# Kernel tuning notes

Hardware: AMD Instinct MI355X
Metric: run time of the kernel (lower is better)

The kernel has to match this reference:

```python
import math
import jax, jax.numpy as jnp
import numpy as np

L, H, D, FF, V, S = 12, 12, 768, 3072, 32000, 1024
HD = D // H
EPS = 1e-5
B, T = 2, 1024


def layernorm(x, w, b):
    mu = jnp.mean(x, axis=-1, keepdims=True)
    var = jnp.mean(jnp.square(x - mu), axis=-1, keepdims=True)
    return (x - mu) * jax.lax.rsqrt(var + EPS) * w + b


def setup_inputs() -> dict:
    key = jax.random.key(0)
    ks = jax.random.split(key, 12)
    std = 0.02
    std_res = 0.02 / math.sqrt(2 * L)  # out_proj / down_proj scaled init
    return {
        "input_ids": jax.random.randint(ks[0], (B, T), 0, V),
        "tok_emb": jax.random.normal(ks[1], (V, D), jnp.float32) * std,
        "pos_emb": jax.random.normal(ks[2], (S, D), jnp.float32) * std,
        "ln1_w": jnp.ones((L, D), jnp.float32),
        "ln1_b": jnp.zeros((L, D), jnp.float32),
        "qkv_w": jax.random.normal(ks[3], (L, 3 * D, D), jnp.float32) * std,
        "out_w": jax.random.normal(ks[4], (L, D, D), jnp.float32) * std_res,
        "ln2_w": jnp.ones((L, D), jnp.float32),
        "ln2_b": jnp.zeros((L, D), jnp.float32),
        "up_w": jax.random.normal(ks[5], (L, FF, D), jnp.float32) * std,
        "down_w": jax.random.normal(ks[6], (L, D, FF), jnp.float32) * std_res,
        "lnf_w": jnp.ones((D,), jnp.float32),
        "lnf_b": jnp.zeros((D,), jnp.float32),
    }


def reference(input_ids, tok_emb, pos_emb, ln1_w, ln1_b, qkv_w, out_w,
              ln2_w, ln2_b, up_w, down_w, lnf_w, lnf_b):
    b, t = input_ids.shape
    x = tok_emb[input_ids] + pos_emb[:t]  # (B,T,D); dropout = eval no-op
    causal = jnp.tril(jnp.ones((t, t), bool))  # (T,T)
    scale = 1.0 / math.sqrt(HD)

    def block(x, p):
        l1w, l1b, qkvw, ow, l2w, l2b, uw, dw = p
        h = layernorm(x, l1w, l1b)
        qkv = h @ qkvw.T  # (B,T,3D)
        q, k, v = jnp.split(qkv, 3, axis=-1)
        q = q.reshape(b, t, H, HD)
        k = k.reshape(b, t, H, HD)
        v = v.reshape(b, t, H, HD)
        scores = jnp.einsum('bihd,bjhd->bhij', q, k) * scale
        scores = jnp.where(causal, scores, -jnp.inf)
        probs = jax.nn.softmax(scores, axis=-1)  # attn_dropout = eval no-op
        o = jnp.einsum('bhij,bjhd->bihd', probs, v).reshape(b, t, D)
        x = x + o @ ow.T
        h2 = layernorm(x, l2w, l2b)
        x = x + jax.nn.gelu(h2 @ uw.T, approximate=False) @ dw.T
        return x, None

    x, _ = jax.lax.scan(block, x, (ln1_w, ln1_b, qkv_w, out_w, ln2_w, ln2_b, up_w, down_w))
    x = layernorm(x, lnf_w, lnf_b)
    logits = x @ tok_emb.T  # tied lm_head
    return logits
```

## Files before the change

### kernel.cpp

```cpp
#include <hip/hip_runtime.h>
#include <hip/hip_bf16.h>
#include <math.h>

#define L_  12
#define H_  12
#define D_  768
#define FF_ 3072
#define V_  32000
#define T_  1024
#define B_  2
#define BT_ (B_*T_)

typedef unsigned short ushort_t;
typedef unsigned int   uint_t;
typedef __bf16 bf16x8 __attribute__((ext_vector_type(8)));
typedef float  f32x4  __attribute__((ext_vector_type(4)));

__device__ __forceinline__ uint_t f2bf1(float f) {
    uint_t u = __builtin_bit_cast(uint_t, f);
    return (u + 0x7FFFu + ((u >> 16) & 1u)) >> 16;
}
__device__ __forceinline__ uint_t f2bf2(float lo, float hi) {
    return f2bf1(lo) | (f2bf1(hi) << 16);
}

__device__ __forceinline__ void gl_lds16(const ushort_t* g, ushort_t* l) {
    __builtin_amdgcn_global_load_lds(
        (const __attribute__((address_space(1))) uint_t*)g,
        (__attribute__((address_space(3))) uint_t*)l, 16, 0, 0);
}

__global__ __launch_bounds__(256) void cast_bf16(const float* __restrict__ in,
                                                 ushort_t* __restrict__ out, int n8)
{
    for (int i = blockIdx.x * 256 + threadIdx.x; i < n8; i += gridDim.x * 256) {
        const float4* p = (const float4*)(in + (size_t)i * 8);
        float4 a = p[0], b = p[1];
        *(uint4*)(out + (size_t)i * 8) =
            make_uint4(f2bf2(a.x,a.y), f2bf2(a.z,a.w), f2bf2(b.x,b.y), f2bf2(b.z,b.w));
    }
}

__global__ __launch_bounds__(256) void cast_layer(const float* __restrict__ q,
    const float* __restrict__ o, const float* __restrict__ u, const float* __restrict__ d,
    ushort_t* __restrict__ out)
{
    const int N0 = 3*D_*D_/8, N1 = N0 + D_*D_/8, N2 = N1 + FF_*D_/8, N3 = N2 + D_*FF_/8;
    for (int i = blockIdx.x * 256 + threadIdx.x; i < N3; i += gridDim.x * 256) {
        const float* src;
        if      (i < N0) src = q + (size_t)i * 8;
        else if (i < N1) src = o + (size_t)(i - N0) * 8;
        else if (i < N2) src = u + (size_t)(i - N1) * 8;
        else             src = d + (size_t)(i - N2) * 8;
        const float4* p = (const float4*)src;
        float4 a = p[0], b = p[1];
        *(uint4*)(out + (size_t)i * 8) =
            make_uint4(f2bf2(a.x,a.y), f2bf2(a.z,a.w), f2bf2(b.x,b.y), f2bf2(b.z,b.w));
    }
}

#define EPI_F32   0
#define EPI_BF16  1
#define EPI_GELU  2
#define EPI_ATOM  3

template <int EPI, int KS>
__global__ __launch_bounds__(256) void gemm_bt(
    const ushort_t* __restrict__ A, const ushort_t* __restrict__ W,
    void* __restrict__ Cv, int N, int K, int Kc)
{
    __shared__ ushort_t As[128 * 64];
    __shared__ ushort_t Bs[128 * 64];

    const int tid  = threadIdx.x;
    const int w    = tid >> 6;
    const int lane = tid & 63;

    const int nwg = gridDim.x;
    int swz = (blockIdx.x & 7) * (nwg >> 3) + (blockIdx.x >> 3);
    const int mt   = swz & 15;
    int rest       = swz >> 4;
    const int ks   = rest & (KS - 1);
    const int nt   = rest / KS;
    const int m0 = mt * 128, n0 = nt * 128;
    const int kb = ks * Kc,  ke = kb + Kc;

    const int srow = lane >> 3;
    const int scol = ((lane & 7) ^ srow) * 8;
    const ushort_t* gA = A + (size_t)(m0 + w * 32 + srow) * K + scol;
    const ushort_t* gW = W + (size_t)(n0 + w * 32 + srow) * K + scol;
    ushort_t* lA = As + w * 2048;
    ushort_t* lB = Bs + w * 2048;
    const size_t row8 = (size_t)8 * K;

    const int lr = lane & 15;
    const int lg = lane >> 4;
    const int wm = (w >> 1) * 64;
    const int wn = (w & 1) * 64;

    f32x4 acc[4][4] = {};

    for (int k0 = kb; k0 < ke; k0 += 64) {
        #pragma unroll
        for (int i = 0; i < 4; ++i) {
            gl_lds16(gA + k0 + i * row8, lA + i * 512);
            gl_lds16(gW + k0 + i * row8, lB + i * 512);
        }
        __syncthreads();

        #pragma unroll
        for (int kk = 0; kk < 2; ++kk) {
            bf16x8 av[4], bv[4];
            #pragma unroll
            for (int i = 0; i < 4; ++i) {
                int rr = wm + i * 16 + lr;
                int ch = (lg + 4 * kk) ^ (rr & 7);
                av[i] = *(const bf16x8*)&As[rr * 64 + ch * 8];
            }
            #pragma unroll
            for (int j = 0; j < 4; ++j) {
                int rr = wn + j * 16 + lr;
                int ch = (lg + 4 * kk) ^ (rr & 7);
                bv[j] = *(const bf16x8*)&Bs[rr * 64 + ch * 8];
            }
            #pragma unroll
            for (int i = 0; i < 4; ++i)
                #pragma unroll
                for (int j = 0; j < 4; ++j)
                    acc[i][j] = __builtin_amdgcn_mfma_f32_16x16x32_bf16(av[i], bv[j], acc[i][j], 0, 0, 0);
        }
        __syncthreads();
    }

    float*    Cf = (float*)Cv;
    ushort_t* Cb = (ushort_t*)Cv;
    const int rbase = (lane >> 4) * 4;
    #pragma unroll
    for (int i = 0; i < 4; ++i) {
        #pragma unroll
        for (int j = 0; j < 4; ++j) {
            #pragma unroll
            for (int r = 0; r < 4; ++r) {
                int row = m0 + wm + i * 16 + rbase + r;
                int col = n0 + wn + j * 16 + lr;
                size_t idx = (size_t)row * N + col;
                float v = acc[i][j][r];
                if (EPI == EPI_F32)  Cf[idx] = v;
                if (EPI == EPI_BF16) Cb[idx] = (ushort_t)f2bf1(v);
                if (EPI == EPI_GELU) Cb[idx] = (ushort_t)f2bf1(0.5f * v * (1.0f + erff(v * 0.70710678118654752f)));
                if (EPI == EPI_ATOM) atomicAdd(&Cf[idx], v);
            }
        }
    }
}

__global__ __launch_bounds__(256) void vprep(const ushort_t* __restrict__ qkv,
                                             ushort_t* __restrict__ vt)
{
    __shared__ ushort_t Vs[64][72];
    const int blk   = blockIdx.x;
    const int ttile = blk & 15;
    const int bh    = blk >> 4;
    const int b     = bh / H_;
    const int h     = bh % H_;
    const int tid   = threadIdx.x;
    const int t0    = ttile * 64;
    {
        const int tr = tid >> 2;
        const int dc = (tid & 3) * 16;
        const uint4* src = (const uint4*)(qkv + (size_t)(b * T_ + t0 + tr) * 2304 + 1536 + h * 64 + dc);
        uint4 v0 = src[0], v1 = src[1];
        *(uint4*)&Vs[tr][dc]     = v0;
        *(uint4*)&Vs[tr][dc + 8] = v1;
    }
    __syncthreads();
    {
        const int d  = tid >> 2;
        const int jc = (tid & 3) * 16;
        uint_t w[8];
        #pragma unroll
        for (int i = 0; i < 8; ++i)
            w[i] = (uint_t)Vs[jc + 2*i][d] | ((uint_t)Vs[jc + 2*i + 1][d] << 16);
        uint4* dst = (uint4*)(vt + ((size_t)bh * 64 + d) * T_ + t0 + jc);
        dst[0] = make_uint4(w[0], w[1], w[2], w[3]);
        dst[1] = make_uint4(w[4], w[5], w[6], w[7]);
    }
}

__global__ __launch_bounds__(64) void attn_mfma(const ushort_t* __restrict__ qkv,
    const ushort_t* __restrict__ vt, ushort_t* __restrict__ o)
{
    __shared__ ushort_t Ps[16 * 136];

    int swz = (blockIdx.x & 7) * 192 + (blockIdx.x >> 3);
    const int bh  = swz >> 6;
    const int qtl = 63 - (swz & 63);
    const int b   = bh / H_;
    const int h   = bh % H_;
    const int lane = threadIdx.x;
    const int l15  = lane & 15;
    const int lg   = lane >> 4;
    const int qbase = qtl * 16;
    const int qlast = qbase + 15;

    const ushort_t* qp = qkv + ((size_t)(b * T_) + qbase + l15) * 2304 + h * 64 + lg * 8;
    bf16x8 qf0 = *(const bf16x8*)qp;
    bf16x8 qf1 = *(const bf16x8*)(qp + 32);

    f32x4 od[4] = {};
    float mr[4] = {-INFINITY, -INFINITY, -INFINITY, -INFINITY};
    float lr[4] = {0.f, 0.f, 0.f, 0.f};

    const ushort_t* kbase = qkv + (size_t)(b * T_) * 2304 + 768 + h * 64;
    const ushort_t* vbase = vt + (size_t)bh * 64 * T_;
    const float SC = 0.18033688011112042f;

    for (int j0 = 0; j0 <= qlast; j0 += 128) {
        f32x4 s[8];
        __builtin_amdgcn_s_setprio(1);
        #pragma unroll
        for (int n = 0; n < 8; ++n) {
            if (j0 + 16 * n <= qlast) {
                const ushort_t* kr = kbase + (size_t)(j0 + 16 * n + l15) * 2304 + lg * 8;
                bf16x8 kf0 = *(const bf16x8*)kr;
                bf16x8 kf1 = *(const bf16x8*)(kr + 32);
                f32x4 a = {};
                a = __builtin_amdgcn_mfma_f32_16x16x32_bf16(qf0, kf0, a, 0, 0, 0);
                a = __builtin_amdgcn_mfma_f32_16x16x32_bf16(qf1, kf1, a, 0, 0, 0);
                s[n] = a;
            } else {
                s[n] = f32x4{-INFINITY, -INFINITY, -INFINITY, -INFINITY};
            }
        }
        __builtin_amdgcn_s_setprio(0);

        #pragma unroll
        for (int n = 0; n < 8; ++n) {
            #pragma unroll
            for (int r = 0; r < 4; ++r) {
                float v = s[n][r] * SC;
                int jg = j0 + 16 * n + l15;
                int qg = qbase + lg * 4 + r;
                if (jg > qg) v = -INFINITY;
                s[n][r] = v;
            }
        }

        float al[4];
        #pragma unroll
        for (int r = 0; r < 4; ++r) {
            float tm = fmaxf(fmaxf(fmaxf(s[0][r], s[1][r]), fmaxf(s[2][r], s[3][r])),
                             fmaxf(fmaxf(s[4][r], s[5][r]), fmaxf(s[6][r], s[7][r])));
            tm = fmaxf(tm, __shfl_xor(tm, 1, 64));
            tm = fmaxf(tm, __shfl_xor(tm, 2, 64));
            tm = fmaxf(tm, __shfl_xor(tm, 4, 64));
            tm = fmaxf(tm, __shfl_xor(tm, 8, 64));
            float mn = fmaxf(mr[r], tm);
            al[r] = exp2f(mr[r] - mn);
            mr[r] = mn;
        }
        #pragma unroll
        for (int n = 0; n < 8; ++n)
            #pragma unroll
            for (int r = 0; r < 4; ++r)
                s[n][r] = exp2f(s[n][r] - mr[r]);
        #pragma unroll
        for (int r = 0; r < 4; ++r) {
            float ps = (s[0][r] + s[1][r]) + (s[2][r] + s[3][r]);
            ps += (s[4][r] + s[5][r]) + (s[6][r] + s[7][r]);
            ps += __shfl_xor(ps, 1, 64);
            ps += __shfl_xor(ps, 2, 64);
            ps += __shfl_xor(ps, 4, 64);
            ps += __shfl_xor(ps, 8, 64);
            lr[r] = lr[r] * al[r] + ps;
        }
        #pragma unroll
        for (int n = 0; n < 4; ++n)
            #pragma unroll
            for (int r = 0; r < 4; ++r)
                od[n][r] *= al[r];

        #pragma unroll
        for (int n = 0; n < 8; ++n)
            #pragma unroll
            for (int r = 0; r < 4; ++r)
                Ps[(lg * 4 + r) * 136 + 16 * n + l15] = (ushort_t)f2bf1(s[n][r]);

        __builtin_amdgcn_s_setprio(1);
        #pragma unroll
        for (int kc = 0; kc < 4; ++kc) {
            if (j0 + kc * 32 <= qlast) {
                bf16x8 pa = *(const bf16x8*)&Ps[l15 * 136 + kc * 32 + lg * 8];
                #pragma unroll
                for (int nn = 0; nn < 4; ++nn) {
                    bf16x8 vf = *(const bf16x8*)&vbase[(size_t)(16 * nn + l15) * T_ + j0 + kc * 32 + lg * 8];
                    od[nn] = __builtin_amdgcn_mfma_f32_16x16x32_bf16(pa, vf, od[nn], 0, 0, 0);
                }
            }
        }
        __builtin_amdgcn_s_setprio(0);
    }

    #pragma unroll
    for (int r = 0; r < 4; ++r) {
        float inv = 1.0f / lr[r];
        int row = qbase + lg * 4 + r;
        ushort_t* op = o + ((size_t)(b * T_ + row)) * 768 + h * 64 + l15;
        #pragma unroll
        for (int nn = 0; nn < 4; ++nn)
            op[16 * nn] = (ushort_t)f2bf1(od[nn][r] * inv);
    }
}

__global__ __launch_bounds__(256) void ln_kernel(const float* __restrict__ x,
    const float* __restrict__ w, const float* __restrict__ bia, ushort_t* __restrict__ out)
{
    const int row = blockIdx.x;
    const int tid = threadIdx.x;
    const float* xr = x + (size_t)row * 768;
    float v0 = xr[tid], v1 = xr[tid + 256], v2 = xr[tid + 512];
    float s  = v0 + v1 + v2;
    float s2 = v0 * v0 + v1 * v1 + v2 * v2;
    #pragma unroll
    for (int off = 32; off > 0; off >>= 1) {
        s  += __shfl_down(s,  off, 64);
        s2 += __shfl_down(s2, off, 64);
    }
    __shared__ float sh[8];
    const int wave = tid >> 6;
    if ((tid & 63) == 0) { sh[wave] = s; sh[4 + wave] = s2; }
    __syncthreads();
    float S  = sh[0] + sh[1] + sh[2] + sh[3];
    float S2 = sh[4] + sh[5] + sh[6] + sh[7];
    float mean = S * (1.f / 768.f);
    float var  = S2 * (1.f / 768.f) - mean * mean;
    float inv  = rsqrtf(var + 1e-5f);
    ushort_t* orow = out + (size_t)row * 768;
    orow[tid]       = (ushort_t)f2bf1((v0 - mean) * inv * w[tid]       + bia[tid]);
    orow[tid + 256] = (ushort_t)f2bf1((v1 - mean) * inv * w[tid + 256] + bia[tid + 256]);
    orow[tid + 512] = (ushort_t)f2bf1((v2 - mean) * inv * w[tid + 512] + bia[tid + 512]);
}

__global__ __launch_bounds__(256) void embed_kernel(const int* __restrict__ ids,
    const float* __restrict__ tok, const float* __restrict__ pos, float* __restrict__ x)
{
    const int bt = blockIdx.x;
    const int t  = bt % T_;
    const int id = ids[bt];
    const int tid = threadIdx.x;
    const float* tr = tok + (size_t)id * 768;
    const float* pr = pos + (size_t)t * 768;
    float* xr = x + (size_t)bt * 768;
    xr[tid]       = tr[tid]       + pr[tid];
    xr[tid + 256] = tr[tid + 256] + pr[tid + 256];
    xr[tid + 512] = tr[tid + 512] + pr[tid + 512];
}

extern "C" void kernel_launch(void* const* d_in, const int* in_sizes, int n_in,
                              void* d_out, int out_size, void* d_ws, size_t ws_size,
                              hipStream_t stream)
{
    const int*   ids   = (const int*)  d_in[0];
    const float* tok   = (const float*)d_in[1];
    const float* pos   = (const float*)d_in[2];
    const float* ln1w  = (const float*)d_in[3];
    const float* ln1b  = (const float*)d_in[4];
    const float* qkvw  = (const float*)d_in[5];
    const float* outw  = (const float*)d_in[6];
    const float* ln2w  = (const float*)d_in[7];
    const float* ln2b  = (const float*)d_in[8];
    const float* upw   = (const float*)d_in[9];
    const float* downw = (const float*)d_in[10];
    const float* lnfw  = (const float*)d_in[11];
    const float* lnfb  = (const float*)d_in[12];
    float* out = (float*)d_out;

    char* ws = (char*)d_ws;
    ushort_t* h    = (ushort_t*)ws;
    float*    x    = (float*)   (ws + 3145728);
    ushort_t* qkv  = (ushort_t*)(ws + 9437184);
    ushort_t* o    = qkv  + (size_t)BT_ * 3 * D_;
    ushort_t* vt   = o    + (size_t)BT_ * D_;
    ushort_t* ffh  = vt   + (size_t)B_ * H_ * 64 * T_;
    ushort_t* layerW = ffh + (size_t)BT_ * FF_;
    ushort_t* tokW = (ushort_t*)(ws + 3145728);

    ushort_t* qkvwB  = layerW;
    ushort_t* outwB  = qkvwB + (size_t)3 * D_ * D_;
    ushort_t* upwB   = outwB + (size_t)D_ * D_;
    ushort_t* downwB = upwB  + (size_t)FF_ * D_;

    embed_kernel<<<BT_, 256, 0, stream>>>(ids, tok, pos, x);

    for (int l = 0; l < L_; ++l) {
        cast_layer<<<1024, 256, 0, stream>>>(
            qkvw  + (size_t)l * 3 * D_ * D_,
            outw  + (size_t)l * D_ * D_,
            upw   + (size_t)l * FF_ * D_,
            downw + (size_t)l * D_ * FF_, layerW);

        ln_kernel<<<BT_, 256, 0, stream>>>(x, ln1w + l * D_, ln1b + l * D_, h);

        gemm_bt<EPI_BF16, 1><<<16 * (3 * D_ / 128), 256, 0, stream>>>(
            h, qkvwB, qkv, 3 * D_, D_, D_);

        vprep<<<B_ * H_ * (T_ / 64), 256, 0, stream>>>(qkv, vt);
        attn_mfma<<<B_ * H_ * (T_ / 16), 64, 0, stream>>>(qkv, vt, o);

        gemm_bt<EPI_ATOM, 2><<<16 * (D_ / 128) * 2, 256, 0, stream>>>(
            o, outwB, x, D_, D_, D_ / 2);

        ln_kernel<<<BT_, 256, 0, stream>>>(x, ln2w + l * D_, ln2b + l * D_, h);

        gemm_bt<EPI_GELU, 1><<<16 * (FF_ / 128), 256, 0, stream>>>(
            h, upwB, ffh, FF_, D_, D_);

        gemm_bt<EPI_ATOM, 4><<<16 * (D_ / 128) * 4, 256, 0, stream>>>(
            ffh, downwB, x, D_, FF_, FF_ / 4);
    }

    ln_kernel<<<BT_, 256, 0, stream>>>(x, lnfw, lnfb, h);
    cast_bf16<<<2048, 256, 0, stream>>>(tok, tokW, V_ * D_ / 8);
    gemm_bt<EPI_F32, 1><<<16 * (V_ / 128), 256, 0, stream>>>(
        h, tokW, out, V_, D_, D_);
}
```

Before: 2.195 ms.

## Double-buffer GEMM LDS tiles and replace split-K atomics with BM=64 residual epilogue

The GEMM kernel now double-buffers its LDS tiles, so the next K-slice is prefetched while MFMAs run on the current one. It also raises wave priority around the MFMA block. The out-projection and down-projection GEMMs drop split-K with atomicAdd and instead use a 64-row M tile with a plain residual-add store, which keeps enough workgroups in flight. This removes atomic traffic and the serialized load-then-compute pattern, at the cost of twice the LDS per block and one fewer wave of split-K parallelism on the long-K down-projection.

```diff
diff --git a/kernel.cpp b/kernel.cpp
--- a/kernel.cpp
+++ b/kernel.cpp
@@ -62,15 +62,18 @@
 #define EPI_F32   0
 #define EPI_BF16  1
 #define EPI_GELU  2
-#define EPI_ATOM  3
-
-template <int EPI, int KS>
+#define EPI_RES   3
+
+template <int EPI, int BM>
 __global__ __launch_bounds__(256) void gemm_bt(
     const ushort_t* __restrict__ A, const ushort_t* __restrict__ W,
-    void* __restrict__ Cv, int N, int K, int Kc)
-{
-    __shared__ ushort_t As[128 * 64];
-    __shared__ ushort_t Bs[128 * 64];
+    const float* R, void* Cv, int N, int K)
+{
+    constexpr int MI = BM / 32;
+    constexpr int AH = BM * 64;
+    constexpr int BH = 128 * 64;
+    __shared__ ushort_t As[2 * AH];
+    __shared__ ushort_t Bs[2 * BH];
 
     const int tid  = threadIdx.x;
     const int w    = tid >> 6;
@@ -78,65 +81,74 @@
 
     const int nwg = gridDim.x;
     int swz = (blockIdx.x & 7) * (nwg >> 3) + (blockIdx.x >> 3);
-    const int mt   = swz & 15;
-    int rest       = swz >> 4;
-    const int ks   = rest & (KS - 1);
-    const int nt   = rest / KS;
-    const int m0 = mt * 128, n0 = nt * 128;
-    const int kb = ks * Kc,  ke = kb + Kc;
+    constexpr int MT = 2048 / BM;
+    const int mt = swz & (MT - 1);
+    const int nt = swz / MT;
+    const int m0 = mt * BM, n0 = nt * 128;
 
     const int srow = lane >> 3;
     const int scol = ((lane & 7) ^ srow) * 8;
-    const ushort_t* gA = A + (size_t)(m0 + w * 32 + srow) * K + scol;
+    const ushort_t* gA = A + (size_t)(m0 + w * (BM / 4) + srow) * K + scol;
     const ushort_t* gW = W + (size_t)(n0 + w * 32 + srow) * K + scol;
-    ushort_t* lA = As + w * 2048;
-    ushort_t* lB = Bs + w * 2048;
     const size_t row8 = (size_t)8 * K;
 
     const int lr = lane & 15;
     const int lg = lane >> 4;
-    const int wm = (w >> 1) * 64;
+    const int wm = (w >> 1) * (BM / 2);
     const int wn = (w & 1) * 64;
 
-    f32x4 acc[4][4] = {};
-
-    for (int k0 = kb; k0 < ke; k0 += 64) {
-        #pragma unroll
-        for (int i = 0; i < 4; ++i) {
+    f32x4 acc[MI][4] = {};
+
+    auto stage = [&](int buf, int k0) {
+        ushort_t* lA = As + buf * AH + w * (BM / 4) * 64;
+        ushort_t* lB = Bs + buf * BH + w * 2048;
+        #pragma unroll
+        for (int i = 0; i < BM / 32; ++i)
             gl_lds16(gA + k0 + i * row8, lA + i * 512);
+        #pragma unroll
+        for (int i = 0; i < 4; ++i)
             gl_lds16(gW + k0 + i * row8, lB + i * 512);
-        }
-        __syncthreads();
-
+    };
+
+    stage(0, 0);
+    __syncthreads();
+    int cur = 0;
+    for (int k0 = 0; k0 < K; k0 += 64) {
+        if (k0 + 64 < K) stage(cur ^ 1, k0 + 64);
+        const ushort_t* Ab = As + cur * AH;
+        const ushort_t* Bb = Bs + cur * BH;
+        __builtin_amdgcn_s_setprio(1);
         #pragma unroll
         for (int kk = 0; kk < 2; ++kk) {
-            bf16x8 av[4], bv[4];
-            #pragma unroll
-            for (int i = 0; i < 4; ++i) {
+            bf16x8 av[MI], bv[4];
+            #pragma unroll
+            for (int i = 0; i < MI; ++i) {
                 int rr = wm + i * 16 + lr;
                 int ch = (lg + 4 * kk) ^ (rr & 7);
-                av[i] = *(const bf16x8*)&As[rr * 64 + ch * 8];
+                av[i] = *(const bf16x8*)&Ab[rr * 64 + ch * 8];
             }
             #pragma unroll
             for (int j = 0; j < 4; ++j) {
                 int rr = wn + j * 16 + lr;
                 int ch = (lg + 4 * kk) ^ (rr & 7);
-                bv[j] = *(const bf16x8*)&Bs[rr * 64 + ch * 8];
-            }
-            #pragma unroll
-            for (int i = 0; i < 4; ++i)
+                bv[j] = *(const bf16x8*)&Bb[rr * 64 + ch * 8];
+            }
+            #pragma unroll
+            for (int i = 0; i < MI; ++i)
                 #pragma unroll
                 for (int j = 0; j < 4; ++j)
                     acc[i][j] = __builtin_amdgcn_mfma_f32_16x16x32_bf16(av[i], bv[j], acc[i][j], 0, 0, 0);
         }
+        __builtin_amdgcn_s_setprio(0);
         __syncthreads();
+        cur ^= 1;
     }
 
     float*    Cf = (float*)Cv;
     ushort_t* Cb = (ushort_t*)Cv;
-    const int rbase = (lane >> 4) * 4;
+    const int rbase = lg * 4;
     #pragma unroll
-    for (int i = 0; i < 4; ++i) {
+    for (int i = 0; i < MI; ++i) {
         #pragma unroll
         for (int j = 0; j < 4; ++j) {
             #pragma unroll
@@ -148,7 +160,7 @@
                 if (EPI == EPI_F32)  Cf[idx] = v;
                 if (EPI == EPI_BF16) Cb[idx] = (ushort_t)f2bf1(v);
                 if (EPI == EPI_GELU) Cb[idx] = (ushort_t)f2bf1(0.5f * v * (1.0f + erff(v * 0.70710678118654752f)));
-                if (EPI == EPI_ATOM) atomicAdd(&Cf[idx], v);
+                if (EPI == EPI_RES)  Cf[idx] = R[idx] + v;
             }
         }
     }
@@ -401,26 +413,26 @@
 
         ln_kernel<<<BT_, 256, 0, stream>>>(x, ln1w + l * D_, ln1b + l * D_, h);
 
-        gemm_bt<EPI_BF16, 1><<<16 * (3 * D_ / 128), 256, 0, stream>>>(
-            h, qkvwB, qkv, 3 * D_, D_, D_);
+        gemm_bt<EPI_BF16, 128><<<16 * (3 * D_ / 128), 256, 0, stream>>>(
+            h, qkvwB, nullptr, qkv, 3 * D_, D_);
 
         vprep<<<B_ * H_ * (T_ / 64), 256, 0, stream>>>(qkv, vt);
         attn_mfma<<<B_ * H_ * (T_ / 16), 64, 0, stream>>>(qkv, vt, o);
 
-        gemm_bt<EPI_ATOM, 2><<<16 * (D_ / 128) * 2, 256, 0, stream>>>(
-            o, outwB, x, D_, D_, D_ / 2);
+        gemm_bt<EPI_RES, 64><<<32 * (D_ / 128), 256, 0, stream>>>(
+            o, outwB, x, x, D_, D_);
 
         ln_kernel<<<BT_, 256, 0, stream>>>(x, ln2w + l * D_, ln2b + l * D_, h);
 
-        gemm_bt<EPI_GELU, 1><<<16 * (FF_ / 128), 256, 0, stream>>>(
-            h, upwB, ffh, FF_, D_, D_);
-
-        gemm_bt<EPI_ATOM, 4><<<16 * (D_ / 128) * 4, 256, 0, stream>>>(
-            ffh, downwB, x, D_, FF_, FF_ / 4);
+        gemm_bt<EPI_GELU, 128><<<16 * (FF_ / 128), 256, 0, stream>>>(
+            h, upwB, nullptr, ffh, FF_, D_);
+
+        gemm_bt<EPI_RES, 64><<<32 * (D_ / 128), 256, 0, stream>>>(
+            ffh, downwB, x, x, D_, FF_);
     }
 
     ln_kernel<<<BT_, 256, 0, stream>>>(x, lnfw, lnfb, h);
     cast_bf16<<<2048, 256, 0, stream>>>(tok, tokW, V_ * D_ / 8);
-    gemm_bt<EPI_F32, 1><<<16 * (V_ / 128), 256, 0, stream>>>(
-        h, tokW, out, V_, D_, D_);
-}
+    gemm_bt<EPI_F32, 128><<<16 * (V_ / 128), 256, 0, stream>>>(
+        h, tokW, nullptr, out, V_, D_);
+}
```

Result: slower. 2.328 ms (+6.1%).
